# Kernel tuning notes

Measured on AMD Instinct MI355X. Metric: run time of the kernel, lower is better.

Reference implementation:

```python
import jax, jax.numpy as jnp
import numpy as np

BN = 100000
E = 1600000
C1 = 64
C2 = 64


def setup_inputs() -> dict:
    key = jax.random.key(0)
    k1, k2, k3, k4 = jax.random.split(key, 4)
    x = jax.random.normal(k1, (BN, C1), dtype=jnp.float32)
    e_ = jax.random.randint(k2, (2, E), 0, BN, dtype=jnp.int64)
    # nn.Linear(C1, C2): y = x @ W^T + b; store W pre-transposed as (C1, C2)
    W = jax.random.normal(k3, (C1, C2), dtype=jnp.float32) * (1.0 / np.sqrt(C1))
    b = jax.random.normal(k4, (C2,), dtype=jnp.float32) * 0.01
    return {"x": x, "e_": e_, "W": W, "b": b}


def reference(x, e_, W, b):
    bn = x.shape[0]
    row, col = e_[0], e_[1]
    # deg = bincount(row); deg^{-1/2} with inf -> 0
    deg = jax.ops.segment_sum(jnp.ones(row.shape, dtype=x.dtype), row, num_segments=bn)
    deg_inv_sqrt = jnp.where(deg > 0, jnp.power(jnp.maximum(deg, 1.0), -0.5), 0.0)
    norm = deg_inv_sqrt[row] * deg_inv_sqrt[col]          # (E,)
    h = x @ W + b                                         # (BN, C2)
    messages = norm[:, None] * h[row]                     # (E, C2) gather + scale
    y = jax.ops.segment_sum(messages, col, num_segments=bn)  # scatter-add over dst
    return y
```

## Files before the change

### kernel.cpp

```cpp
#include <hip/hip_runtime.h>
#include <hip/hip_bf16.h>

#define C 64
#define CPB 256
#define NBUCK 391
#define EPB 4096
#define PAD 16
#define CAP 5120

typedef __attribute__((ext_vector_type(8))) short bf16x8;
typedef __attribute__((ext_vector_type(4))) float f32x4;

__device__ __forceinline__ unsigned short f2bf(float f) {
    __hip_bfloat16 h = __float2bfloat16(f);
    return *(unsigned short*)&h;
}

__global__ __launch_bounds__(256) void partA_kernel(const int* __restrict__ row,
                                                    const int* __restrict__ col,
                                                    int* __restrict__ bcurC,
                                                    int* __restrict__ bcurR,
                                                    int* __restrict__ stageC,
                                                    unsigned char* __restrict__ stageR,
                                                    int ne) {
    __shared__ int cC[NBUCK], cR[NBUCK];
    const int tid = threadIdx.x;
    for (int i = tid; i < NBUCK; i += 256) { cC[i] = 0; cR[i] = 0; }
    __syncthreads();
    const int s = blockIdx.x * EPB, e = min(s + EPB, ne);
    int rr[16], cc[16];
#pragma unroll
    for (int u = 0; u < 16; ++u) {
        int i = s + tid + u * 256;
        if (i < e) { rr[u] = row[i]; cc[u] = col[i]; }
        else { rr[u] = -1; cc[u] = -1; }
    }
#pragma unroll
    for (int u = 0; u < 16; ++u) {
        if (cc[u] >= 0) {
            atomicAdd(&cC[cc[u] >> 8], 1);
            atomicAdd(&cR[rr[u] >> 8], 1);
        }
    }
    __syncthreads();
    for (int t = tid; t < NBUCK; t += 256) {
        int g = atomicAdd(&bcurC[t * PAD], cC[t]); cC[t] = t * CAP + g;
        g = atomicAdd(&bcurR[t * PAD], cR[t]);     cR[t] = t * CAP + g;
    }
    __syncthreads();
#pragma unroll
    for (int u = 0; u < 16; ++u) {
        if (cc[u] >= 0) {
            int bk = cc[u] >> 8;
            int pos = atomicAdd(&cC[bk], 1);
            if (pos < (bk + 1) * CAP) stageC[pos] = ((cc[u] & 255) << 17) | rr[u];
            int rb = rr[u] >> 8;
            int posR = atomicAdd(&cR[rb], 1);
            if (posR < (rb + 1) * CAP) stageR[posR] = (unsigned char)(rr[u] & 255);
        }
    }
}

__global__ __launch_bounds__(512) void fusedB_kernel(const int* __restrict__ bcC,
                                                     const int* __restrict__ bcR,
                                                     const int* __restrict__ stageC,
                                                     const unsigned char* __restrict__ stageR,
                                                     float* __restrict__ dis,
                                                     int* __restrict__ offs,
                                                     int* __restrict__ srcs,
                                                     int bn, int ne) {
    __shared__ int hist[CPB];
    __shared__ int wv8[8];
    __shared__ int wsum[4];
    __shared__ int sbase_s;
    const int b = blockIdx.x, tid = threadIdx.x;
    const int lane = tid & 63, wid = tid >> 6;

    if (tid < CPB) hist[tid] = 0;
    __syncthreads();
    const int sbR = b * CAP;
    const int cntR = min(bcR[b * PAD], CAP);
    for (int j = tid; j < cntR; j += 512) atomicAdd(&hist[stageR[sbR + j]], 1);
    __syncthreads();
    {
        int r = b * CPB + tid;
        if (tid < CPB && r < bn) {
            int d = hist[tid];
            dis[r] = d > 0 ? rsqrtf((float)d) : 0.0f;
        }
    }
    int part = 0;
    for (int t = tid; t < b; t += 512) part += min(bcC[t * PAD], CAP);
#pragma unroll
    for (int off = 32; off >= 1; off >>= 1) part += __shfl_xor(part, off, 64);
    if (lane == 0) wv8[wid] = part;
    __syncthreads();
    if (tid == 0) {
        int s = 0;
#pragma unroll
        for (int k = 0; k < 8; ++k) s += wv8[k];
        sbase_s = s;
    }
    __syncthreads();
    const int sbase = sbase_s;
    if (tid < CPB) hist[tid] = 0;
    __syncthreads();
    const int sbC = b * CAP;
    const int cntC = min(bcC[b * PAD], CAP);
    for (int j = tid; j < cntC; j += 512) atomicAdd(&hist[stageC[sbC + j] >> 17], 1);
    __syncthreads();
    int v = 0, x = 0;
    if (tid < CPB) {
        v = hist[tid];
        x = v;
#pragma unroll
        for (int off = 1; off < 64; off <<= 1) {
            int t = __shfl_up(x, off, 64);
            if (lane >= off) x += t;
        }
        if (lane == 63) wsum[wid] = x;
    }
    __syncthreads();
    if (tid == 0) {
        int a = 0;
#pragma unroll
        for (int k = 0; k < 4; ++k) { int t = wsum[k]; wsum[k] = a; a += t; }
    }
    __syncthreads();
    if (tid < CPB) {
        int excl = (x - v) + wsum[wid];
        int c = b * CPB + tid;
        if (c < bn) offs[c] = sbase + excl;
        hist[tid] = sbase + excl;
    }
    __syncthreads();
    for (int j = tid; j < cntC; j += 512) {
        int val = stageC[sbC + j];
        int pos = atomicAdd(&hist[val >> 17], 1);
        srcs[pos] = val & 0x1FFFF;
    }
    if (b == NBUCK - 1 && tid == 0) offs[bn] = sbase + cntC;
}

__global__ __launch_bounds__(256) void linear_mfma_kernel(const float* __restrict__ x,
                                                          const float* __restrict__ W,
                                                          const float* __restrict__ b,
                                                          const float* __restrict__ dis,
                                                          __hip_bfloat16* __restrict__ hb,
                                                          int bn) {
    __shared__ unsigned short xb[64][72];
    __shared__ unsigned short Wt[64][72];
    __shared__ float bs[64];
    __shared__ float dss[64];
    const int t = threadIdx.x;
    const int R0 = blockIdx.x * 64;

    {
        int row = t >> 2, q = t & 3;
        int grow = R0 + row;
        float4 vv[4];
        if (grow < bn) {
            const float4* xp = (const float4*)(x + (size_t)grow * C + q * 16);
#pragma unroll
            for (int i = 0; i < 4; ++i) vv[i] = xp[i];
        } else {
#pragma unroll
            for (int i = 0; i < 4; ++i) vv[i] = make_float4(0.f, 0.f, 0.f, 0.f);
        }
#pragma unroll
        for (int i = 0; i < 4; ++i) {
            unsigned short* d = &xb[row][q * 16 + i * 4];
            d[0] = f2bf(vv[i].x); d[1] = f2bf(vv[i].y);
            d[2] = f2bf(vv[i].z); d[3] = f2bf(vv[i].w);
        }
    }
    {
        int k = t >> 2, q = t & 3;
        const float* wp = W + (size_t)k * C + q * 16;
#pragma unroll
        for (int j = 0; j < 16; ++j) Wt[q * 16 + j][k] = f2bf(wp[j]);
    }
    if (t < 64) bs[t] = b[t];
    else if (t < 128) { int i = t - 64; int g = R0 + i; dss[i] = (g < bn) ? dis[g] : 0.f; }
    __syncthreads();

    const int wv = t >> 6;
    const int l = t & 63;
    const int lm = l & 15;
    const int g = l >> 4;

    const bf16x8 a0 = *(const bf16x8*)&xb[wv * 16 + lm][g * 8];
    const bf16x8 a1 = *(const bf16x8*)&xb[wv * 16 + lm][32 + g * 8];

#pragma unroll
    for (int n = 0; n < 4; ++n) {
        const bf16x8 b0 = *(const bf16x8*)&Wt[n * 16 + lm][g * 8];
        const bf16x8 b1 = *(const bf16x8*)&Wt[n * 16 + lm][32 + g * 8];
        float bias = bs[n * 16 + lm];
        f32x4 acc = {bias, bias, bias, bias};
        acc = __builtin_amdgcn_mfma_f32_16x16x32_bf16(a0, b0, acc, 0, 0, 0);
        acc = __builtin_amdgcn_mfma_f32_16x16x32_bf16(a1, b1, acc, 0, 0, 0);
#pragma unroll
        for (int reg = 0; reg < 4; ++reg) {
            int lrow = wv * 16 + g * 4 + reg;
            int grow = R0 + lrow;
            if (grow < bn)
                hb[(size_t)grow * C + n * 16 + lm] = __float2bfloat16(dss[lrow] * acc[reg]);
        }
    }
}

__device__ __forceinline__ float bf_lo(unsigned int p) { return __uint_as_float(p << 16); }
__device__ __forceinline__ float bf_hi(unsigned int p) { return __uint_as_float(p & 0xFFFF0000u); }

__global__ void gather_kernel(const int* __restrict__ offs, const int* __restrict__ srcs,
                              const uint2* __restrict__ hb64,
                              const float* __restrict__ dis,
                              float* __restrict__ y, int bn) {
    int r = blockIdx.x * (blockDim.x >> 6) + (threadIdx.x >> 6);
    if (r >= bn) return;
    const int lane = threadIdx.x & 63;
    const int q = lane >> 4;
    const int cq = lane & 15;
    const int s0 = offs[r], e0 = offs[r + 1];
    float4 acc = {0.f, 0.f, 0.f, 0.f};
    for (int base = s0; base < e0; base += 64) {
        int j = base + lane;
        int srcv = (j < e0) ? srcs[j] : 0;
        int cnt = min(64, e0 - base);
        int t = 0;
        for (; t + 16 <= cnt; t += 16) {
            int a0 = __shfl(srcv, t + q, 64);
            int a1 = __shfl(srcv, t + 4 + q, 64);
            int a2 = __shfl(srcv, t + 8 + q, 64);
            int a3 = __shfl(srcv, t + 12 + q, 64);
            uint2 p0 = hb64[(size_t)a0 * 16 + cq];
            uint2 p1 = hb64[(size_t)a1 * 16 + cq];
            uint2 p2 = hb64[(size_t)a2 * 16 + cq];
            uint2 p3 = hb64[(size_t)a3 * 16 + cq];
            acc.x += bf_lo(p0.x); acc.y += bf_hi(p0.x); acc.z += bf_lo(p0.y); acc.w += bf_hi(p0.y);
            acc.x += bf_lo(p1.x); acc.y += bf_hi(p1.x); acc.z += bf_lo(p1.y); acc.w += bf_hi(p1.y);
            acc.x += bf_lo(p2.x); acc.y += bf_hi(p2.x); acc.z += bf_lo(p2.y); acc.w += bf_hi(p2.y);
            acc.x += bf_lo(p3.x); acc.y += bf_hi(p3.x); acc.z += bf_lo(p3.y); acc.w += bf_hi(p3.y);
        }
        for (; t + 4 <= cnt; t += 4) {
            int a = __shfl(srcv, t + q, 64);
            uint2 p = hb64[(size_t)a * 16 + cq];
            acc.x += bf_lo(p.x); acc.y += bf_hi(p.x); acc.z += bf_lo(p.y); acc.w += bf_hi(p.y);
        }
        if (t < cnt) {
            int idx = t + q;
            int a = __shfl(srcv, idx & 63, 64);
            if (idx < cnt) {
                uint2 p = hb64[(size_t)a * 16 + cq];
                acc.x += bf_lo(p.x); acc.y += bf_hi(p.x); acc.z += bf_lo(p.y); acc.w += bf_hi(p.y);
            }
        }
    }
    acc.x += __shfl_xor(acc.x, 16, 64); acc.y += __shfl_xor(acc.y, 16, 64);
    acc.z += __shfl_xor(acc.z, 16, 64); acc.w += __shfl_xor(acc.w, 16, 64);
    acc.x += __shfl_xor(acc.x, 32, 64); acc.y += __shfl_xor(acc.y, 32, 64);
    acc.z += __shfl_xor(acc.z, 32, 64); acc.w += __shfl_xor(acc.w, 32, 64);
    if (q == 0) {
        float d = dis[r];
        float4 out = {acc.x * d, acc.y * d, acc.z * d, acc.w * d};
        *reinterpret_cast<float4*>(y + (size_t)r * C + 4 * cq) = out;
    }
}

extern "C" void kernel_launch(void* const* d_in, const int* in_sizes, int n_in,
                              void* d_out, int out_size, void* d_ws, size_t ws_size,
                              hipStream_t stream) {
    const float* x = (const float*)d_in[0];
    const int*   e = (const int*)d_in[1];
    const float* W = (const float*)d_in[2];
    const float* b = (const float*)d_in[3];
    float* y = (float*)d_out;

    const int bn = in_sizes[0] / C;
    const int ne = in_sizes[1] / 2;

    const int* rowi = e;
    const int* coli = e + ne;

    char* ws = (char*)d_ws;
    float* dis   = (float*)ws;  ws += (size_t)bn * 4;
    int*   offs  = (int*)ws;    ws += ((size_t)bn + 4) * 4;
    int*   bcC   = (int*)ws;    ws += (size_t)NBUCK * PAD * 4;
    int*   bcR   = (int*)ws;    ws += (size_t)NBUCK * PAD * 4;
    int*   srcs  = (int*)ws;    ws += (size_t)ne * 4;
    int*           stageC = (int*)ws;           ws += (size_t)NBUCK * CAP * 4;
    unsigned char* stageR = (unsigned char*)ws; ws += (size_t)NBUCK * CAP;
    __hip_bfloat16* hb = (__hip_bfloat16*)ws;

    hipMemsetAsync(bcC, 0, (size_t)NBUCK * PAD * 8, stream);

    const int nchunks = (ne + EPB - 1) / EPB;
    partA_kernel<<<nchunks, 256, 0, stream>>>(rowi, coli, bcC, bcR, stageC, stageR, ne);
    fusedB_kernel<<<NBUCK, 512, 0, stream>>>(bcC, bcR, stageC, stageR, dis, offs, srcs, bn, ne);
    linear_mfma_kernel<<<(bn + 63) / 64, 256, 0, stream>>>(x, W, b, dis, hb, bn);
    gather_kernel<<<(bn + 3) / 4, 256, 0, stream>>>(offs, srcs, (const uint2*)hb, dis, y, bn);
}
```

Before: 126.8 us.

## Stage bucketed edges in LDS for coalesced writes; coarser row buckets

The partition kernel now sorts each chunk's edges by bucket in shared memory, then writes them out contiguously using a binary search over the bucket offsets. This replaces the scattered per-edge global stores. The degree (row) buckets become 1024 nodes wide with 16-bit local indices, so there are fewer buckets, and the chunk size doubles to 8192 edges with 512 threads. The change adds two local prefix scans, extra barriers and per-element binary searches. It also leaves fewer, larger blocks doing the degree histogram in the second kernel.

Measured after the change: 123.9 us. -2.3%, faster.

```diff
diff --git a/kernel.cpp b/kernel.cpp
--- a/kernel.cpp
+++ b/kernel.cpp
@@ -3,10 +3,13 @@
 
 #define C 64
 #define CPB 256
-#define NBUCK 391
-#define EPB 4096
+#define NBUCKC 391
+#define CAPC 5120
+#define RPB 1024
+#define NBUCKR 98
+#define CAPR 20480
+#define EPB 8192
 #define PAD 16
-#define CAP 5120
 
 typedef __attribute__((ext_vector_type(8))) short bf16x8;
 typedef __attribute__((ext_vector_type(4))) float f32x4;
@@ -16,22 +19,38 @@
     return *(unsigned short*)&h;
 }
 
-__global__ __launch_bounds__(256) void partA_kernel(const int* __restrict__ row,
+__device__ __forceinline__ int seg_find(const int* seg, int n, int i) {
+    int lo = 0, hi = n;
+    while (hi - lo > 1) {
+        int mid = (lo + hi) >> 1;
+        if (seg[mid] <= i) lo = mid; else hi = mid;
+    }
+    return lo;
+}
+
+__global__ __launch_bounds__(512) void partA_kernel(const int* __restrict__ row,
                                                     const int* __restrict__ col,
                                                     int* __restrict__ bcurC,
                                                     int* __restrict__ bcurR,
                                                     int* __restrict__ stageC,
-                                                    unsigned char* __restrict__ stageR,
+                                                    unsigned short* __restrict__ stageR,
                                                     int ne) {
-    __shared__ int cC[NBUCK], cR[NBUCK];
+    __shared__ int buf[EPB];
+    __shared__ int cC[NBUCKC], segC[NBUCKC + 1], dC[NBUCKC];
+    __shared__ int cR[NBUCKR], segR[NBUCKR + 1], dR[NBUCKR];
     const int tid = threadIdx.x;
-    for (int i = tid; i < NBUCK; i += 256) { cC[i] = 0; cR[i] = 0; }
-    __syncthreads();
+    const int lane = tid & 63, wid = tid >> 6;
+
+    for (int i = tid; i < NBUCKC; i += 512) cC[i] = 0;
+    if (tid < NBUCKR) cR[tid] = 0;
+    __syncthreads();
+
     const int s = blockIdx.x * EPB, e = min(s + EPB, ne);
+    const int nloc = e - s;
     int rr[16], cc[16];
 #pragma unroll
     for (int u = 0; u < 16; ++u) {
-        int i = s + tid + u * 256;
+        int i = s + tid + u * 512;
         if (i < e) { rr[u] = row[i]; cc[u] = col[i]; }
         else { rr[u] = -1; cc[u] = -1; }
     }
@@ -39,58 +58,117 @@
     for (int u = 0; u < 16; ++u) {
         if (cc[u] >= 0) {
             atomicAdd(&cC[cc[u] >> 8], 1);
-            atomicAdd(&cR[rr[u] >> 8], 1);
-        }
-    }
-    __syncthreads();
-    for (int t = tid; t < NBUCK; t += 256) {
-        int g = atomicAdd(&bcurC[t * PAD], cC[t]); cC[t] = t * CAP + g;
-        g = atomicAdd(&bcurR[t * PAD], cR[t]);     cR[t] = t * CAP + g;
+            atomicAdd(&cR[rr[u] >> 10], 1);
+        }
+    }
+    __syncthreads();
+    if (wid == 0) {
+        int carry = 0;
+        for (int base = 0; base < NBUCKC; base += 64) {
+            int idx = base + lane;
+            int v = (idx < NBUCKC) ? cC[idx] : 0;
+            int x = v;
+#pragma unroll
+            for (int off = 1; off < 64; off <<= 1) {
+                int t = __shfl_up(x, off, 64);
+                if (lane >= off) x += t;
+            }
+            if (idx < NBUCKC) segC[idx] = carry + x - v;
+            carry += __shfl(x, 63, 64);
+        }
+        if (lane == 0) segC[NBUCKC] = carry;
+    } else if (wid == 1) {
+        int carry = 0;
+        for (int base = 0; base < NBUCKR; base += 64) {
+            int idx = base + lane;
+            int v = (idx < NBUCKR) ? cR[idx] : 0;
+            int x = v;
+#pragma unroll
+            for (int off = 1; off < 64; off <<= 1) {
+                int t = __shfl_up(x, off, 64);
+                if (lane >= off) x += t;
+            }
+            if (idx < NBUCKR) segR[idx] = carry + x - v;
+            carry += __shfl(x, 63, 64);
+        }
+        if (lane == 0) segR[NBUCKR] = carry;
+    }
+    __syncthreads();
+    for (int t = tid; t < NBUCKC; t += 512) {
+        int cnt = cC[t];
+        dC[t] = t * CAPC + atomicAdd(&bcurC[t * PAD], cnt) - segC[t];
+        cC[t] = segC[t];
+    }
+    if (tid < NBUCKR) {
+        int cnt = cR[tid];
+        dR[tid] = tid * CAPR + atomicAdd(&bcurR[tid * PAD], cnt) - segR[tid];
+        cR[tid] = segR[tid];
     }
     __syncthreads();
 #pragma unroll
     for (int u = 0; u < 16; ++u) {
         if (cc[u] >= 0) {
             int bk = cc[u] >> 8;
-            int pos = atomicAdd(&cC[bk], 1);
-            if (pos < (bk + 1) * CAP) stageC[pos] = ((cc[u] & 255) << 17) | rr[u];
-            int rb = rr[u] >> 8;
-            int posR = atomicAdd(&cR[rb], 1);
-            if (posR < (rb + 1) * CAP) stageR[posR] = (unsigned char)(rr[u] & 255);
-        }
+            int lpos = atomicAdd(&cC[bk], 1);
+            buf[lpos] = ((cc[u] & 255) << 17) | rr[u];
+        }
+    }
+    __syncthreads();
+    for (int i = tid; i < nloc; i += 512) {
+        int b = seg_find(segC, NBUCKC, i);
+        int dst = dC[b] + i;
+        if (dst < (b + 1) * CAPC) stageC[dst] = buf[i];
+    }
+    __syncthreads();
+#pragma unroll
+    for (int u = 0; u < 16; ++u) {
+        if (rr[u] >= 0) {
+            int rb = rr[u] >> 10;
+            int lpos = atomicAdd(&cR[rb], 1);
+            buf[lpos] = rr[u];
+        }
+    }
+    __syncthreads();
+    for (int i = tid; i < nloc; i += 512) {
+        int b = seg_find(segR, NBUCKR, i);
+        int dst = dR[b] + i;
+        if (dst < (b + 1) * CAPR) stageR[dst] = (unsigned short)(buf[i] & (RPB - 1));
     }
 }
 
 __global__ __launch_bounds__(512) void fusedB_kernel(const int* __restrict__ bcC,
                                                      const int* __restrict__ bcR,
                                                      const int* __restrict__ stageC,
-                                                     const unsigned char* __restrict__ stageR,
+                                                     const unsigned short* __restrict__ stageR,
                                                      float* __restrict__ dis,
                                                      int* __restrict__ offs,
                                                      int* __restrict__ srcs,
                                                      int bn, int ne) {
     __shared__ int hist[CPB];
+    __shared__ int dhist[RPB];
     __shared__ int wv8[8];
     __shared__ int wsum[4];
     __shared__ int sbase_s;
     const int b = blockIdx.x, tid = threadIdx.x;
     const int lane = tid & 63, wid = tid >> 6;
 
-    if (tid < CPB) hist[tid] = 0;
-    __syncthreads();
-    const int sbR = b * CAP;
-    const int cntR = min(bcR[b * PAD], CAP);
-    for (int j = tid; j < cntR; j += 512) atomicAdd(&hist[stageR[sbR + j]], 1);
-    __syncthreads();
-    {
-        int r = b * CPB + tid;
-        if (tid < CPB && r < bn) {
-            int d = hist[tid];
-            dis[r] = d > 0 ? rsqrtf((float)d) : 0.0f;
+    if (b < NBUCKR) {
+        for (int i = tid; i < RPB; i += 512) dhist[i] = 0;
+        __syncthreads();
+        const int sbR = b * CAPR;
+        const int cntR = min(bcR[b * PAD], CAPR);
+        for (int j = tid; j < cntR; j += 512) atomicAdd(&dhist[stageR[sbR + j]], 1);
+        __syncthreads();
+        for (int i = tid; i < RPB; i += 512) {
+            int r = b * RPB + i;
+            if (r < bn) {
+                int d = dhist[i];
+                dis[r] = d > 0 ? rsqrtf((float)d) : 0.0f;
+            }
         }
     }
     int part = 0;
-    for (int t = tid; t < b; t += 512) part += min(bcC[t * PAD], CAP);
+    for (int t = tid; t < b; t += 512) part += min(bcC[t * PAD], CAPC);
 #pragma unroll
     for (int off = 32; off >= 1; off >>= 1) part += __shfl_xor(part, off, 64);
     if (lane == 0) wv8[wid] = part;
@@ -101,12 +179,11 @@
         for (int k = 0; k < 8; ++k) s += wv8[k];
         sbase_s = s;
     }
+    if (tid < CPB) hist[tid] = 0;
     __syncthreads();
     const int sbase = sbase_s;
-    if (tid < CPB) hist[tid] = 0;
-    __syncthreads();
-    const int sbC = b * CAP;
-    const int cntC = min(bcC[b * PAD], CAP);
+    const int sbC = b * CAPC;
+    const int cntC = min(bcC[b * PAD], CAPC);
     for (int j = tid; j < cntC; j += 512) atomicAdd(&hist[stageC[sbC + j] >> 17], 1);
     __syncthreads();
     int v = 0, x = 0;
@@ -139,7 +216,7 @@
         int pos = atomicAdd(&hist[val >> 17], 1);
         srcs[pos] = val & 0x1FFFF;
     }
-    if (b == NBUCK - 1 && tid == 0) offs[bn] = sbase + cntC;
+    if (b == NBUCKC - 1 && tid == 0) offs[bn] = sbase + cntC;
 }
 
 __global__ __launch_bounds__(256) void linear_mfma_kernel(const float* __restrict__ x,
@@ -286,18 +363,18 @@
     char* ws = (char*)d_ws;
     float* dis   = (float*)ws;  ws += (size_t)bn * 4;
     int*   offs  = (int*)ws;    ws += ((size_t)bn + 4) * 4;
-    int*   bcC   = (int*)ws;    ws += (size_t)NBUCK * PAD * 4;
-    int*   bcR   = (int*)ws;    ws += (size_t)NBUCK * PAD * 4;
+    int*   bcC   = (int*)ws;    ws += (size_t)NBUCKC * PAD * 4;
+    int*   bcR   = (int*)ws;    ws += (size_t)NBUCKR * PAD * 4;
     int*   srcs  = (int*)ws;    ws += (size_t)ne * 4;
-    int*           stageC = (int*)ws;           ws += (size_t)NBUCK * CAP * 4;
-    unsigned char* stageR = (unsigned char*)ws; ws += (size_t)NBUCK * CAP;
+    int*            stageC = (int*)ws;            ws += (size_t)NBUCKC * CAPC * 4;
+    unsigned short* stageR = (unsigned short*)ws; ws += (size_t)NBUCKR * CAPR * 2;
     __hip_bfloat16* hb = (__hip_bfloat16*)ws;
 
-    hipMemsetAsync(bcC, 0, (size_t)NBUCK * PAD * 8, stream);
+    hipMemsetAsync(bcC, 0, (size_t)(NBUCKC + NBUCKR) * PAD * 4, stream);
 
     const int nchunks = (ne + EPB - 1) / EPB;
-    partA_kernel<<<nchunks, 256, 0, stream>>>(rowi, coli, bcC, bcR, stageC, stageR, ne);
-    fusedB_kernel<<<NBUCK, 512, 0, stream>>>(bcC, bcR, stageC, stageR, dis, offs, srcs, bn, ne);
+    partA_kernel<<<nchunks, 512, 0, stream>>>(rowi, coli, bcC, bcR, stageC, stageR, ne);
+    fusedB_kernel<<<NBUCKC, 512, 0, stream>>>(bcC, bcR, stageC, stageR, dis, offs, srcs, bn, ne);
     linear_mfma_kernel<<<(bn + 63) / 64, 256, 0, stream>>>(x, W, b, dis, hb, bn);
     gather_kernel<<<(bn + 3) / 4, 256, 0, stream>>>(offs, srcs, (const uint2*)hb, dis, y, bn);
 }
```
